# Kernel optimization log

Measured on AMD Instinct MI355X. Metric: run time of the kernel, lower is better.

Reference implementation:

```python
import jax, jax.numpy as jnp
import numpy as np

B, L, H, F = 8, 1024, 512, 4

def setup_inputs() -> dict:
    key = jax.random.key(0)
    ks = jax.random.split(key, 5)
    x = jax.random.normal(ks[0], (B, L, H), dtype=jnp.float32)
    x_mask = jax.random.randint(ks[1], (B, L), 0, 2).astype(jnp.int32)
    W_proj = jax.random.normal(ks[2], (H, H * F), dtype=jnp.float32) * (1.0 / np.sqrt(H))
    b_proj = jnp.zeros((H * F,), dtype=jnp.float32)
    W_gate = jax.random.normal(ks[3], (2 * H, 2 * H), dtype=jnp.float32) * (1.0 / np.sqrt(2 * H))
    b_gate = jnp.zeros((2 * H,), dtype=jnp.float32)
    return {"x": x, "x_mask": x_mask, "W_proj": W_proj, "b_proj": b_proj,
            "W_gate": W_gate, "b_gate": b_gate}

def masked_softmax(logits, mask, eps=1e-13):
    # allennlp-style masked softmax used throughout sgnlp:
    # softmax(logits * mask) * mask, renormalized.
    m = mask.astype(logits.dtype)
    p = jax.nn.softmax(logits * m, axis=-1) * m
    return p / (p.sum(axis=-1, keepdims=True) + eps)

def reference(x, x_mask, W_proj, b_proj, W_gate, b_gate):
    b, l, h = x.shape
    # multi-factor projection: (B,L,H) -> (B,L,H,F) with relu (Linear activation='relu', dropout=0)
    y = jax.nn.relu(jnp.einsum('blh,hk->blk', x, W_proj) + b_proj)
    y = y.reshape(b, l, h, F)
    # per-factor self-attn scores stacked on last axis: (B,L,L,F)
    scores = jnp.einsum('blhf,bmhf->blmf', y, y)
    self_attn = scores.max(axis=-1)  # attn_pooling == 'max'
    # pairwise mask, zero diagonal
    mask = x_mask[:, :, None] * x_mask[:, None, :]
    mask = mask * (1 - jnp.eye(l, dtype=mask.dtype))
    alpha = masked_softmax(self_attn, mask)
    multi_attn_enc = jnp.einsum('blm,bmh->blh', alpha, x)
    joint = jnp.concatenate([x, multi_attn_enc], axis=-1)  # (B,L,2H)
    gate = jax.nn.sigmoid(jnp.einsum('blk,kj->blj', joint, W_gate) + b_gate)
    return gate * joint
```

## Files before the change

### kernel.cpp

```cpp
#include <hip/hip_runtime.h>


typedef _Float16 half8 __attribute__((ext_vector_type(8)));
typedef float floatx4 __attribute__((ext_vector_type(4)));

typedef const __attribute__((address_space(1))) void* gas_ptr;
typedef __attribute__((address_space(3))) void* las_ptr;


template<int NCH, int NT>
__device__ __forceinline__ void init_ptrs(const _Float16* src, int row0, int ld,
                                          const _Float16* gp[NCH]) {
  int t = threadIdx.x;
#pragma unroll
  for (int p = 0; p < NCH; ++p) {
    int c = p * NT + t;
    int row = c >> 3;
    int kg = c & 7;
    int gk = (kg ^ (row & 7)) << 3;
    gp[p] = src + (size_t)(row0 + row) * ld + gk;
  }
}

template<int NCH, int NT>
__device__ __forceinline__ void stage(const _Float16* const gp[NCH], _Float16* ldsbuf) {
  int t = threadIdx.x;
#pragma unroll
  for (int p = 0; p < NCH; ++p)
    __builtin_amdgcn_global_load_lds((gas_ptr)gp[p],
                                     (las_ptr)(ldsbuf + t * 8 + p * NT * 8), 16, 0, 0);
}

template<int NCH>
__device__ __forceinline__ void bump(const _Float16* gp[NCH], int d) {
#pragma unroll
  for (int p = 0; p < NCH; ++p) gp[p] += d;
}

__device__ __forceinline__ half8 frag_ld(const _Float16* lds, int row, int g) {
  return *(const half8*)(lds + row * 64 + ((g ^ (row & 7)) << 3));
}

__device__ __forceinline__ void mfma_tile44(const _Float16* lds_a, const _Float16* lds_b,
                                            floatx4 acc[4][4], int wm, int wn,
                                            int l16, int quad) {
#pragma unroll
  for (int kf = 0; kf < 2; ++kf) {
    half8 af[4], bf[4];
#pragma unroll
    for (int i = 0; i < 4; ++i) af[i] = frag_ld(lds_a, wm * 64 + i * 16 + l16, kf * 4 + quad);
#pragma unroll
    for (int i = 0; i < 4; ++i) bf[i] = frag_ld(lds_b, wn * 64 + i * 16 + l16, kf * 4 + quad);
#pragma unroll
    for (int mi = 0; mi < 4; ++mi)
#pragma unroll
      for (int ni = 0; ni < 4; ++ni)
        acc[mi][ni] = __builtin_amdgcn_mfma_f32_16x16x32_f16(af[mi], bf[ni], acc[mi][ni], 0, 0, 0);
  }
}

#define ZERO_ACC44(acc)                                 \
  _Pragma("unroll") for (int mi = 0; mi < 4; ++mi)      \
  _Pragma("unroll") for (int ni = 0; ni < 4; ++ni)      \
  _Pragma("unroll") for (int r = 0; r < 4; ++r) acc[mi][ni][r] = 0.0f;

__device__ __forceinline__ void mfma_tile42(const _Float16* la, const _Float16* lb,
                                            floatx4 acc[4][2], int wm, int wn,
                                            int l16, int quad) {
#pragma unroll
  for (int kf = 0; kf < 2; ++kf) {
    half8 af[4], bf[2];
#pragma unroll
    for (int i = 0; i < 4; ++i) af[i] = frag_ld(la, wm * 64 + i * 16 + l16, kf * 4 + quad);
#pragma unroll
    for (int i = 0; i < 2; ++i) bf[i] = frag_ld(lb, wn * 32 + i * 16 + l16, kf * 4 + quad);
#pragma unroll
    for (int mi = 0; mi < 4; ++mi)
#pragma unroll
      for (int ni = 0; ni < 2; ++ni)
        acc[mi][ni] = __builtin_amdgcn_mfma_f32_16x16x32_f16(af[mi], bf[ni], acc[mi][ni], 0, 0, 0);
  }
}

#define ZERO_ACC42(acc)                                 \
  _Pragma("unroll") for (int mi = 0; mi < 4; ++mi)      \
  _Pragma("unroll") for (int ni = 0; ni < 2; ++ni)      \
  _Pragma("unroll") for (int r = 0; r < 4; ++r) acc[mi][ni][r] = 0.0f;


__global__ void x_prep_kernel(const float* __restrict__ in, _Float16* __restrict__ x16,
                              _Float16* __restrict__ xT) {
  __shared__ float tile[32][33];
  const int R = 1024, C = 512;
  int c0 = blockIdx.y * 32, r0 = blockIdx.z * 32;
  size_t boff = (size_t)blockIdx.x * R * C;
  in += boff; x16 += boff; xT += boff;
  int tx = threadIdx.x & 31, ty = threadIdx.x >> 5;
#pragma unroll
  for (int i = 0; i < 32; i += 8) {
    float v = in[(size_t)(r0 + ty + i) * C + c0 + tx];
    tile[ty + i][tx] = v;
    x16[(size_t)(r0 + ty + i) * C + c0 + tx] = (_Float16)v;
  }
  __syncthreads();
#pragma unroll
  for (int i = 0; i < 32; i += 8)
    xT[(size_t)(c0 + ty + i) * R + r0 + tx] = (_Float16)tile[tx][ty + i];
}

__global__ void w_prep_kernel(const float* __restrict__ Wp, _Float16* __restrict__ WpT,
                              const float* __restrict__ Wg, _Float16* __restrict__ WgT) {
  __shared__ float tile[32][33];
  const float* in; _Float16* out; int R, C, c0, r0;
  if (blockIdx.z == 0) {
    in = Wp; out = WpT; R = 512; C = 2048;
    c0 = blockIdx.x * 32; r0 = blockIdx.y * 32;
  } else {
    in = Wg; out = WgT; R = 1024; C = 1024;
    c0 = (blockIdx.x & 31) * 32; r0 = (blockIdx.y * 2 + (blockIdx.x >> 5)) * 32;
  }
  int tx = threadIdx.x & 31, ty = threadIdx.x >> 5;
#pragma unroll
  for (int i = 0; i < 32; i += 8)
    tile[ty + i][tx] = in[(size_t)(r0 + ty + i) * C + c0 + tx];
  __syncthreads();
#pragma unroll
  for (int i = 0; i < 32; i += 8) {
    int rr = c0 + ty + i;
    int prow = (blockIdx.z == 0) ? ((rr & 3) * 512 + (rr >> 2)) : rr;
    out[(size_t)prow * R + r0 + tx] = (_Float16)tile[tx][ty + i];
  }
}


__global__ __launch_bounds__(256) void proj_kernel(const _Float16* __restrict__ x16,
                                                   const _Float16* __restrict__ WpT,
                                                   const float* __restrict__ bp,
                                                   _Float16* __restrict__ y_t) {
  __shared__ __align__(16) _Float16 ldsA[2][128 * 64];
  __shared__ __align__(16) _Float16 ldsB[2][128 * 64];
  int id = blockIdx.x;
  int xcd = id & 7, r = id >> 3;
  int i0 = (xcd * 8 + (r & 7)) * 128;
  int n0 = (r >> 3) * 128;
  int t = threadIdx.x, lane = t & 63, w = t >> 6;
  int wm = w >> 1, wn = w & 1, quad = lane >> 4, l16 = lane & 15;
  const _Float16* gpA[4]; const _Float16* gpB[4];
  init_ptrs<4, 256>(x16, i0, 512, gpA);
  init_ptrs<4, 256>(WpT, n0, 512, gpB);
  floatx4 acc[4][4];
  ZERO_ACC44(acc);
  stage<4, 256>(gpA, ldsA[0]); bump<4>(gpA, 64);
  stage<4, 256>(gpB, ldsB[0]); bump<4>(gpB, 64);
#pragma unroll 1
  for (int kt = 0; kt < 8; ++kt) {
    __syncthreads();
    if (kt < 7) {
      stage<4, 256>(gpA, ldsA[(kt + 1) & 1]); bump<4>(gpA, 64);
      stage<4, 256>(gpB, ldsB[(kt + 1) & 1]); bump<4>(gpB, 64);
    }
    mfma_tile44(ldsA[kt & 1], ldsB[kt & 1], acc, wm, wn, l16, quad);
  }
#pragma unroll
  for (int mi = 0; mi < 4; ++mi)
#pragma unroll
    for (int ni = 0; ni < 4; ++ni)
#pragma unroll
      for (int r2 = 0; r2 < 4; ++r2) {
        int gr = i0 + wm * 64 + mi * 16 + quad * 4 + r2;
        int gc = n0 + wn * 64 + ni * 16 + l16;
        int f = gc >> 9, h = gc & 511;
        float c = fmaxf(acc[mi][ni][r2] + bp[h * 4 + f], 0.0f);
        int b = gr >> 10, l = gr & 1023;
        y_t[(((size_t)(b * 4 + f)) * 1024 + l) * 512 + h] = (_Float16)c;
      }
}


__global__ __launch_bounds__(256, 3) void score_kernel(const _Float16* __restrict__ y_t,
                                                       float* __restrict__ S) {
  __shared__ __align__(16) char smem[49152];
  _Float16* LA0 = (_Float16*)smem;
  _Float16* LA1 = (_Float16*)(smem + 16384);
  _Float16* LB0 = (_Float16*)(smem + 32768);
  _Float16* LB1 = (_Float16*)(smem + 40960);
  int id = blockIdx.x;
  int b = id & 7;
  int tt = id >> 3;
  int ti = 0;
  while (tt >= 16 - 2 * ti) { tt -= 16 - 2 * ti; ++ti; }
  int jh = 2 * ti + tt;
  int i0 = ti * 128, j0 = jh * 64;
  int t = threadIdx.x, lane = t & 63, w = t >> 6;
  int wm = w >> 1, wn = w & 1, quad = lane >> 4, l16 = lane & 15;
  const int PLANE = 1024 * 512;
  const _Float16* base = y_t + (size_t)b * 4 * PLANE;
  const _Float16* gpA[4]; const _Float16* gpB[2];
  init_ptrs<4, 256>(base, i0, 512, gpA);
  init_ptrs<2, 256>(base, j0, 512, gpB);
  floatx4 acc[4][2], smax[4][2];
  ZERO_ACC42(acc);
  stage<4, 256>(gpA, LA0); bump<4>(gpA, 64);
  stage<2, 256>(gpB, LB0); bump<2>(gpB, 64);
#pragma unroll 1
  for (int f = 0; f < 4; ++f) {
#pragma unroll 1
    for (int kt = 0; kt < 8; ++kt) {
      __syncthreads();
      if (f * 8 + kt < 31) {
        if (kt == 7) { bump<4>(gpA, PLANE - 512); bump<2>(gpB, PLANE - 512); }
        stage<4, 256>(gpA, ((kt + 1) & 1) ? LA1 : LA0); bump<4>(gpA, 64);
        stage<2, 256>(gpB, ((kt + 1) & 1) ? LB1 : LB0); bump<2>(gpB, 64);
      }
      mfma_tile42((kt & 1) ? LA1 : LA0, (kt & 1) ? LB1 : LB0, acc, wm, wn, l16, quad);
    }
    if (f == 0) {
#pragma unroll
      for (int mi = 0; mi < 4; ++mi)
#pragma unroll
        for (int ni = 0; ni < 2; ++ni) smax[mi][ni] = acc[mi][ni];
    } else {
#pragma unroll
      for (int mi = 0; mi < 4; ++mi)
#pragma unroll
        for (int ni = 0; ni < 2; ++ni)
#pragma unroll
          for (int r = 0; r < 4; ++r)
            smax[mi][ni][r] = fmaxf(smax[mi][ni][r], acc[mi][ni][r]);
    }
    ZERO_ACC42(acc);
  }
  float* Sb = S + (size_t)b * 1024 * 1024;
#pragma unroll
  for (int mi = 0; mi < 4; ++mi)
#pragma unroll
    for (int ni = 0; ni < 2; ++ni)
#pragma unroll
      for (int r = 0; r < 4; ++r) {
        int gi = i0 + wm * 64 + mi * 16 + quad * 4 + r;
        int gj = j0 + wn * 32 + ni * 16 + l16;
        Sb[(size_t)gi * 1024 + gj] = smax[mi][ni][r];
      }
  if (jh >= 2 * ti + 2) {
    __syncthreads();
    float* tl = (float*)smem;
#pragma unroll
    for (int mi = 0; mi < 4; ++mi)
#pragma unroll
      for (int ni = 0; ni < 2; ++ni)
#pragma unroll
        for (int r = 0; r < 4; ++r)
          tl[(wm * 64 + mi * 16 + quad * 4 + r) * 65 + (wn * 32 + ni * 16 + l16)] =
              smax[mi][ni][r];
    __syncthreads();
#pragma unroll 1
    for (int k = 0; k < 32; ++k) {
      int flat = k * 256 + t;
      int rm = flat >> 7, cm = flat & 127;
      Sb[(size_t)(j0 + rm) * 1024 + (i0 + cm)] = tl[cm * 65 + rm];
    }
  }
}


__global__ __launch_bounds__(256) void softmax_kernel(const float* __restrict__ S,
                                                      const int* __restrict__ xmask,
                                                      _Float16* __restrict__ alpha) {
  __shared__ float red[16];
  int id = blockIdx.x;
  int b = id & 7, l = id >> 3;
  int row = b * 1024 + l;
  const float* sr = S + (size_t)row * 1024;
  const int* mr = xmask + b * 1024;
  int t = threadIdx.x, lane = t & 63, wid = t >> 6;
  int rm = mr[l];
  float v[4], mm[4];
  float vmax = 0.0f;
#pragma unroll
  for (int q = 0; q < 4; ++q) {
    int i = t + q * 256;
    int m = (rm && mr[i] && (i != l)) ? 1 : 0;
    mm[q] = (float)m;
    v[q] = m ? sr[i] : 0.0f;
    vmax = fmaxf(vmax, v[q]);
  }
  for (int off = 32; off; off >>= 1) vmax = fmaxf(vmax, __shfl_down(vmax, off));
  if (lane == 0) red[wid] = vmax;
  __syncthreads();
  if (t == 0) red[8] = fmaxf(fmaxf(red[0], red[1]), fmaxf(red[2], red[3]));
  __syncthreads();
  vmax = red[8];
  float e[4], E = 0.0f, E2 = 0.0f;
#pragma unroll
  for (int q = 0; q < 4; ++q) {
    e[q] = expf(v[q] - vmax);
    E += e[q];
    E2 += e[q] * mm[q];
  }
  for (int off = 32; off; off >>= 1) {
    E += __shfl_down(E, off);
    E2 += __shfl_down(E2, off);
  }
  if (lane == 0) { red[wid] = E; red[4 + wid] = E2; }
  __syncthreads();
  if (t == 0) {
    red[9] = red[0] + red[1] + red[2] + red[3];
    red[10] = red[4] + red[5] + red[6] + red[7];
  }
  __syncthreads();
  E = red[9]; E2 = red[10];
  float inv = 1.0f / (E2 + 1e-13f * E);
  _Float16* ar = alpha + (size_t)row * 1024;
#pragma unroll
  for (int q = 0; q < 4; ++q) {
    int i = t + q * 256;
    ar[i] = (_Float16)(e[q] * mm[q] * inv);
  }
}


__global__ __launch_bounds__(256) void attn_kernel(const _Float16* __restrict__ alpha,
                                                   const _Float16* __restrict__ xT,
                                                   _Float16* __restrict__ enc) {
  __shared__ __align__(16) _Float16 ldsA[2][64 * 64];
  __shared__ __align__(16) _Float16 ldsB[2][128 * 64];
  int id = blockIdx.x;
  int b = id & 7;
  int r2 = id >> 3;
  int i0 = (r2 >> 2) * 64;
  int n0 = (r2 & 3) * 128;
  const _Float16* A = alpha + (size_t)b * 1024 * 1024;
  const _Float16* Bm = xT + (size_t)b * 512 * 1024;
  int t = threadIdx.x, lane = t & 63, wn = t >> 6;
  int quad = lane >> 4, l16 = lane & 15;
  const _Float16* gpA[2]; const _Float16* gpB[4];
  init_ptrs<2, 256>(A, i0, 1024, gpA);
  init_ptrs<4, 256>(Bm, n0, 1024, gpB);
  floatx4 acc[4][2];
  ZERO_ACC42(acc);
  stage<2, 256>(gpA, ldsA[0]); bump<2>(gpA, 64);
  stage<4, 256>(gpB, ldsB[0]); bump<4>(gpB, 64);
#pragma unroll 1
  for (int kt = 0; kt < 16; ++kt) {
    __syncthreads();
    if (kt < 15) {
      stage<2, 256>(gpA, ldsA[(kt + 1) & 1]); bump<2>(gpA, 64);
      stage<4, 256>(gpB, ldsB[(kt + 1) & 1]); bump<4>(gpB, 64);
    }
    const _Float16* la = ldsA[kt & 1];
    const _Float16* lb = ldsB[kt & 1];
#pragma unroll
    for (int kf = 0; kf < 2; ++kf) {
      half8 af[4], bf[2];
#pragma unroll
      for (int i = 0; i < 4; ++i) af[i] = frag_ld(la, i * 16 + l16, kf * 4 + quad);
#pragma unroll
      for (int i = 0; i < 2; ++i) bf[i] = frag_ld(lb, wn * 32 + i * 16 + l16, kf * 4 + quad);
#pragma unroll
      for (int mi = 0; mi < 4; ++mi)
#pragma unroll
        for (int ni = 0; ni < 2; ++ni)
          acc[mi][ni] = __builtin_amdgcn_mfma_f32_16x16x32_f16(af[mi], bf[ni], acc[mi][ni], 0, 0, 0);
    }
  }
  _Float16* eb = enc + (size_t)b * 1024 * 512;
#pragma unroll
  for (int mi = 0; mi < 4; ++mi)
#pragma unroll
    for (int ni = 0; ni < 2; ++ni)
#pragma unroll
      for (int r = 0; r < 4; ++r) {
        int gr = i0 + mi * 16 + quad * 4 + r;
        int gc = n0 + wn * 32 + ni * 16 + l16;
        eb[(size_t)gr * 512 + gc] = (_Float16)acc[mi][ni][r];
      }
}


__global__ __launch_bounds__(256) void gate_kernel(const _Float16* __restrict__ x16,
                                                   const _Float16* __restrict__ enc,
                                                   const _Float16* __restrict__ WgT,
                                                   const float* __restrict__ bg,
                                                   float* __restrict__ out) {
  __shared__ __align__(16) _Float16 ldsA[2][128 * 64];
  __shared__ __align__(16) _Float16 ldsB[2][128 * 64];
  int id = blockIdx.x;
  int xcd = id & 7, r = id >> 3;
  int i0 = (xcd * 8 + (r & 7)) * 128;
  int n0 = (r >> 3) * 128;
  int t = threadIdx.x, lane = t & 63, w = t >> 6;
  int wm = w >> 1, wn = w & 1, quad = lane >> 4, l16 = lane & 15;
  const _Float16* gpA[4]; const _Float16* gpA2[4]; const _Float16* gpB[4];
  init_ptrs<4, 256>(x16, i0, 512, gpA);
  init_ptrs<4, 256>(enc, i0, 512, gpA2);
  init_ptrs<4, 256>(WgT, n0, 1024, gpB);
  floatx4 acc[4][4];
  ZERO_ACC44(acc);
  stage<4, 256>(gpA, ldsA[0]); bump<4>(gpA, 64);
  stage<4, 256>(gpB, ldsB[0]); bump<4>(gpB, 64);
#pragma unroll 1
  for (int kt = 0; kt < 16; ++kt) {
    __syncthreads();
    if (kt < 15) {
      if (kt < 7) { stage<4, 256>(gpA,  ldsA[(kt + 1) & 1]); bump<4>(gpA, 64); }
      else        { stage<4, 256>(gpA2, ldsA[(kt + 1) & 1]); bump<4>(gpA2, 64); }
      stage<4, 256>(gpB, ldsB[(kt + 1) & 1]); bump<4>(gpB, 64);
    }
    mfma_tile44(ldsA[kt & 1], ldsB[kt & 1], acc, wm, wn, l16, quad);
  }
#pragma unroll
  for (int mi = 0; mi < 4; ++mi)
#pragma unroll
    for (int ni = 0; ni < 4; ++ni)
#pragma unroll
      for (int r2 = 0; r2 < 4; ++r2) {
        int gr = i0 + wm * 64 + mi * 16 + quad * 4 + r2;
        int gc = n0 + wn * 64 + ni * 16 + l16;
        float c = acc[mi][ni][r2] + bg[gc];
        float g = 1.0f / (1.0f + expf(-c));
        float jv = (gc < 512) ? (float)x16[(size_t)gr * 512 + gc]
                              : (float)enc[(size_t)gr * 512 + (gc - 512)];
        out[(size_t)gr * 1024 + gc] = g * jv;
      }
}


extern "C" void kernel_launch(void* const* d_in, const int* in_sizes, int n_in,
                              void* d_out, int out_size, void* d_ws, size_t ws_size,
                              hipStream_t stream) {
  const float* x  = (const float*)d_in[0];
  const int* xm   = (const int*)d_in[1];
  const float* Wp = (const float*)d_in[2];
  const float* bp = (const float*)d_in[3];
  const float* Wg = (const float*)d_in[4];
  const float* bg = (const float*)d_in[5];
  float* out = (float*)d_out;

  char* ws = (char*)d_ws;
  const size_t MB = 1024 * 1024;
  _Float16* x16 = (_Float16*)(ws);
  _Float16* xT  = (_Float16*)(ws + 8 * MB);
  _Float16* WpT = (_Float16*)(ws + 16 * MB);
  _Float16* WgT = (_Float16*)(ws + 18 * MB);
  _Float16* y_t = (_Float16*)(ws + 20 * MB);
  float*    S   = (float*)(ws + 52 * MB);
  _Float16* alpha = (_Float16*)(ws + 20 * MB);
  _Float16* enc   = (_Float16*)(ws + 36 * MB);

  x_prep_kernel<<<dim3(8, 16, 32), 256, 0, stream>>>(x, x16, xT);
  w_prep_kernel<<<dim3(64, 16, 2), 256, 0, stream>>>(Wp, WpT, Wg, WgT);

  proj_kernel<<<1024, 256, 0, stream>>>(x16, WpT, bp, y_t);
  score_kernel<<<576, 256, 0, stream>>>(y_t, S);
  softmax_kernel<<<8192, 256, 0, stream>>>(S, xm, alpha);
  attn_kernel<<<512, 256, 0, stream>>>(alpha, xT, enc);
  gate_kernel<<<512, 256, 0, stream>>>(x16, enc, WgT, bg, out);
}
```

Baseline: 203.0 us.

## Deepen proj/gate GEMM pipelines to 4-stage K=32 buffers and merge prep kernels

The proj and gate GEMMs move from a double-buffered K=64 LDS scheme to a four-buffer K=32 ring with a paired-row swizzle. They use explicit vmcnt waits and raw barriers so up to three tiles of loads stay in flight, and raise MFMA priority with setprio during compute. The two preprocessing kernels are merged into one launch. This aims to hide global-load latency and cut one launch. In exchange it adds more barriers per K and hand-tuned waitcnt logic that must match the number of outstanding loads.

```diff
diff --git a/kernel.cpp b/kernel.cpp
--- a/kernel.cpp
+++ b/kernel.cpp
@@ -6,6 +6,8 @@
 
 typedef const __attribute__((address_space(1))) void* gas_ptr;
 typedef __attribute__((address_space(3))) void* las_ptr;
+
+#define WAITV(n) asm volatile("s_waitcnt vmcnt(" #n ") lgkmcnt(0)" ::: "memory")
 
 
 template<int NCH, int NT>
@@ -22,6 +24,22 @@
   }
 }
 
+
+template<int NCH, int NT>
+__device__ __forceinline__ void init_ptrs32(const _Float16* src, int row0, int ld,
+                                            const _Float16* gp[NCH]) {
+  int t = threadIdx.x;
+#pragma unroll
+  for (int p = 0; p < NCH; ++p) {
+    int c = p * NT + t;
+    int pair = c >> 3, s = c & 7;
+    int q = s ^ (pair & 7);
+    int row = row0 + pair * 2 + (q >> 2);
+    int gk = (q & 3) << 3;
+    gp[p] = src + (size_t)row * ld + gk;
+  }
+}
+
 template<int NCH, int NT>
 __device__ __forceinline__ void stage(const _Float16* const gp[NCH], _Float16* ldsbuf) {
   int t = threadIdx.x;
@@ -41,20 +59,42 @@
   return *(const half8*)(lds + row * 64 + ((g ^ (row & 7)) << 3));
 }
 
-__device__ __forceinline__ void mfma_tile44(const _Float16* lds_a, const _Float16* lds_b,
-                                            floatx4 acc[4][4], int wm, int wn,
+__device__ __forceinline__ half8 frag_ld32(const _Float16* lds, int row, int kg) {
+  int pair = row >> 1;
+  int slot = (kg | ((row & 1) << 2)) ^ (pair & 7);
+  return *(const half8*)(lds + pair * 64 + slot * 8);
+}
+
+__device__ __forceinline__ void kstep44(const _Float16* la, const _Float16* lb,
+                                        floatx4 (&acc)[4][4], int ra, int rb, int quad) {
+  half8 af[4], bf[4];
+#pragma unroll
+  for (int mi = 0; mi < 4; ++mi) af[mi] = frag_ld32(la, ra + mi * 16, quad);
+#pragma unroll
+  for (int ni = 0; ni < 4; ++ni) bf[ni] = frag_ld32(lb, rb + ni * 16, quad);
+  __builtin_amdgcn_s_setprio(1);
+#pragma unroll
+  for (int mi = 0; mi < 4; ++mi)
+#pragma unroll
+    for (int ni = 0; ni < 4; ++ni)
+      acc[mi][ni] = __builtin_amdgcn_mfma_f32_16x16x32_f16(af[mi], bf[ni], acc[mi][ni], 0, 0, 0);
+  __builtin_amdgcn_s_setprio(0);
+}
+
+__device__ __forceinline__ void mfma_tile42(const _Float16* la, const _Float16* lb,
+                                            floatx4 acc[4][2], int wm, int wn,
                                             int l16, int quad) {
 #pragma unroll
   for (int kf = 0; kf < 2; ++kf) {
-    half8 af[4], bf[4];
-#pragma unroll
-    for (int i = 0; i < 4; ++i) af[i] = frag_ld(lds_a, wm * 64 + i * 16 + l16, kf * 4 + quad);
-#pragma unroll
-    for (int i = 0; i < 4; ++i) bf[i] = frag_ld(lds_b, wn * 64 + i * 16 + l16, kf * 4 + quad);
+    half8 af[4], bf[2];
+#pragma unroll
+    for (int i = 0; i < 4; ++i) af[i] = frag_ld(la, wm * 64 + i * 16 + l16, kf * 4 + quad);
+#pragma unroll
+    for (int i = 0; i < 2; ++i) bf[i] = frag_ld(lb, wn * 32 + i * 16 + l16, kf * 4 + quad);
 #pragma unroll
     for (int mi = 0; mi < 4; ++mi)
 #pragma unroll
-      for (int ni = 0; ni < 4; ++ni)
+      for (int ni = 0; ni < 2; ++ni)
         acc[mi][ni] = __builtin_amdgcn_mfma_f32_16x16x32_f16(af[mi], bf[ni], acc[mi][ni], 0, 0, 0);
   }
 }
@@ -64,103 +104,100 @@
   _Pragma("unroll") for (int ni = 0; ni < 4; ++ni)      \
   _Pragma("unroll") for (int r = 0; r < 4; ++r) acc[mi][ni][r] = 0.0f;
 
-__device__ __forceinline__ void mfma_tile42(const _Float16* la, const _Float16* lb,
-                                            floatx4 acc[4][2], int wm, int wn,
-                                            int l16, int quad) {
-#pragma unroll
-  for (int kf = 0; kf < 2; ++kf) {
-    half8 af[4], bf[2];
-#pragma unroll
-    for (int i = 0; i < 4; ++i) af[i] = frag_ld(la, wm * 64 + i * 16 + l16, kf * 4 + quad);
-#pragma unroll
-    for (int i = 0; i < 2; ++i) bf[i] = frag_ld(lb, wn * 32 + i * 16 + l16, kf * 4 + quad);
-#pragma unroll
-    for (int mi = 0; mi < 4; ++mi)
-#pragma unroll
-      for (int ni = 0; ni < 2; ++ni)
-        acc[mi][ni] = __builtin_amdgcn_mfma_f32_16x16x32_f16(af[mi], bf[ni], acc[mi][ni], 0, 0, 0);
-  }
-}
-
 #define ZERO_ACC42(acc)                                 \
   _Pragma("unroll") for (int mi = 0; mi < 4; ++mi)      \
   _Pragma("unroll") for (int ni = 0; ni < 2; ++ni)      \
   _Pragma("unroll") for (int r = 0; r < 4; ++r) acc[mi][ni][r] = 0.0f;
 
 
-__global__ void x_prep_kernel(const float* __restrict__ in, _Float16* __restrict__ x16,
-                              _Float16* __restrict__ xT) {
+__global__ __launch_bounds__(256) void prep_kernel(const float* __restrict__ xin,
+                                                   _Float16* __restrict__ x16,
+                                                   _Float16* __restrict__ xT,
+                                                   const float* __restrict__ Wp,
+                                                   _Float16* __restrict__ WpT,
+                                                   const float* __restrict__ Wg,
+                                                   _Float16* __restrict__ WgT) {
   __shared__ float tile[32][33];
-  const int R = 1024, C = 512;
-  int c0 = blockIdx.y * 32, r0 = blockIdx.z * 32;
-  size_t boff = (size_t)blockIdx.x * R * C;
-  in += boff; x16 += boff; xT += boff;
+  int id = blockIdx.x;
   int tx = threadIdx.x & 31, ty = threadIdx.x >> 5;
-#pragma unroll
-  for (int i = 0; i < 32; i += 8) {
-    float v = in[(size_t)(r0 + ty + i) * C + c0 + tx];
-    tile[ty + i][tx] = v;
-    x16[(size_t)(r0 + ty + i) * C + c0 + tx] = (_Float16)v;
-  }
-  __syncthreads();
-#pragma unroll
-  for (int i = 0; i < 32; i += 8)
-    xT[(size_t)(c0 + ty + i) * R + r0 + tx] = (_Float16)tile[tx][ty + i];
-}
-
-__global__ void w_prep_kernel(const float* __restrict__ Wp, _Float16* __restrict__ WpT,
-                              const float* __restrict__ Wg, _Float16* __restrict__ WgT) {
-  __shared__ float tile[32][33];
-  const float* in; _Float16* out; int R, C, c0, r0;
-  if (blockIdx.z == 0) {
-    in = Wp; out = WpT; R = 512; C = 2048;
-    c0 = blockIdx.x * 32; r0 = blockIdx.y * 32;
+  if (id < 4096) {
+    const int R = 1024, C = 512;
+    int b = id & 7, rest = id >> 3;
+    int c0 = (rest & 15) * 32, r0 = (rest >> 4) * 32;
+    size_t boff = (size_t)b * R * C;
+    const float* in = xin + boff;
+    _Float16* o16 = x16 + boff;
+    _Float16* oT = xT + boff;
+#pragma unroll
+    for (int i = 0; i < 32; i += 8) {
+      float v = in[(size_t)(r0 + ty + i) * C + c0 + tx];
+      tile[ty + i][tx] = v;
+      o16[(size_t)(r0 + ty + i) * C + c0 + tx] = (_Float16)v;
+    }
+    __syncthreads();
+#pragma unroll
+    for (int i = 0; i < 32; i += 8)
+      oT[(size_t)(c0 + ty + i) * R + r0 + tx] = (_Float16)tile[tx][ty + i];
   } else {
-    in = Wg; out = WgT; R = 1024; C = 1024;
-    c0 = (blockIdx.x & 31) * 32; r0 = (blockIdx.y * 2 + (blockIdx.x >> 5)) * 32;
-  }
-  int tx = threadIdx.x & 31, ty = threadIdx.x >> 5;
-#pragma unroll
-  for (int i = 0; i < 32; i += 8)
-    tile[ty + i][tx] = in[(size_t)(r0 + ty + i) * C + c0 + tx];
-  __syncthreads();
-#pragma unroll
-  for (int i = 0; i < 32; i += 8) {
-    int rr = c0 + ty + i;
-    int prow = (blockIdx.z == 0) ? ((rr & 3) * 512 + (rr >> 2)) : rr;
-    out[(size_t)prow * R + r0 + tx] = (_Float16)tile[tx][ty + i];
-  }
-}
-
-
-__global__ __launch_bounds__(256) void proj_kernel(const _Float16* __restrict__ x16,
-                                                   const _Float16* __restrict__ WpT,
-                                                   const float* __restrict__ bp,
-                                                   _Float16* __restrict__ y_t) {
-  __shared__ __align__(16) _Float16 ldsA[2][128 * 64];
-  __shared__ __align__(16) _Float16 ldsB[2][128 * 64];
+    int w = id - 4096;
+    int bx = w & 63, by = (w >> 6) & 15, bz = w >> 10;
+    const float* in; _Float16* out; int R, C, c0, r0;
+    if (bz == 0) {
+      in = Wp; out = WpT; R = 512; C = 2048;
+      c0 = bx * 32; r0 = by * 32;
+    } else {
+      in = Wg; out = WgT; R = 1024; C = 1024;
+      c0 = (bx & 31) * 32; r0 = (by * 2 + (bx >> 5)) * 32;
+    }
+#pragma unroll
+    for (int i = 0; i < 32; i += 8)
+      tile[ty + i][tx] = in[(size_t)(r0 + ty + i) * C + c0 + tx];
+    __syncthreads();
+#pragma unroll
+    for (int i = 0; i < 32; i += 8) {
+      int rr = c0 + ty + i;
+      int prow = (bz == 0) ? ((rr & 3) * 512 + (rr >> 2)) : rr;
+      out[(size_t)prow * R + r0 + tx] = (_Float16)tile[tx][ty + i];
+    }
+  }
+}
+
+
+__global__ __launch_bounds__(256, 2) void proj_kernel(const _Float16* __restrict__ x16,
+                                                      const _Float16* __restrict__ WpT,
+                                                      const float* __restrict__ bp,
+                                                      _Float16* __restrict__ y_t) {
+  __shared__ __align__(16) _Float16 ldsA[4][128 * 32];
+  __shared__ __align__(16) _Float16 ldsB[4][128 * 32];
   int id = blockIdx.x;
   int xcd = id & 7, r = id >> 3;
   int i0 = (xcd * 8 + (r & 7)) * 128;
   int n0 = (r >> 3) * 128;
   int t = threadIdx.x, lane = t & 63, w = t >> 6;
   int wm = w >> 1, wn = w & 1, quad = lane >> 4, l16 = lane & 15;
-  const _Float16* gpA[4]; const _Float16* gpB[4];
-  init_ptrs<4, 256>(x16, i0, 512, gpA);
-  init_ptrs<4, 256>(WpT, n0, 512, gpB);
+  int ra = wm * 64 + l16, rb = wn * 64 + l16;
+  const _Float16* gpA[2]; const _Float16* gpB[2];
+  init_ptrs32<2, 256>(x16, i0, 512, gpA);
+  init_ptrs32<2, 256>(WpT, n0, 512, gpB);
   floatx4 acc[4][4];
   ZERO_ACC44(acc);
-  stage<4, 256>(gpA, ldsA[0]); bump<4>(gpA, 64);
-  stage<4, 256>(gpB, ldsB[0]); bump<4>(gpB, 64);
+  stage<2, 256>(gpA, ldsA[0]); bump<2>(gpA, 32);
+  stage<2, 256>(gpB, ldsB[0]); bump<2>(gpB, 32);
+  stage<2, 256>(gpA, ldsA[1]); bump<2>(gpA, 32);
+  stage<2, 256>(gpB, ldsB[1]); bump<2>(gpB, 32);
+  stage<2, 256>(gpA, ldsA[2]); bump<2>(gpA, 32);
+  stage<2, 256>(gpB, ldsB[2]); bump<2>(gpB, 32);
 #pragma unroll 1
-  for (int kt = 0; kt < 8; ++kt) {
-    __syncthreads();
-    if (kt < 7) {
-      stage<4, 256>(gpA, ldsA[(kt + 1) & 1]); bump<4>(gpA, 64);
-      stage<4, 256>(gpB, ldsB[(kt + 1) & 1]); bump<4>(gpB, 64);
-    }
-    mfma_tile44(ldsA[kt & 1], ldsB[kt & 1], acc, wm, wn, l16, quad);
-  }
+  for (int u = 0; u < 13; ++u) {
+    WAITV(8);
+    __builtin_amdgcn_s_barrier();
+    stage<2, 256>(gpA, ldsA[(u + 3) & 3]); bump<2>(gpA, 32);
+    stage<2, 256>(gpB, ldsB[(u + 3) & 3]); bump<2>(gpB, 32);
+    kstep44(ldsA[u & 3], ldsB[u & 3], acc, ra, rb, quad);
+  }
+  WAITV(8); __builtin_amdgcn_s_barrier(); kstep44(ldsA[1], ldsB[1], acc, ra, rb, quad);
+  WAITV(4); __builtin_amdgcn_s_barrier(); kstep44(ldsA[2], ldsB[2], acc, ra, rb, quad);
+  WAITV(0); __builtin_amdgcn_s_barrier(); kstep44(ldsA[3], ldsB[3], acc, ra, rb, quad);
 #pragma unroll
   for (int mi = 0; mi < 4; ++mi)
 #pragma unroll
@@ -377,37 +414,45 @@
 }
 
 
-__global__ __launch_bounds__(256) void gate_kernel(const _Float16* __restrict__ x16,
-                                                   const _Float16* __restrict__ enc,
-                                                   const _Float16* __restrict__ WgT,
-                                                   const float* __restrict__ bg,
-                                                   float* __restrict__ out) {
-  __shared__ __align__(16) _Float16 ldsA[2][128 * 64];
-  __shared__ __align__(16) _Float16 ldsB[2][128 * 64];
+__global__ __launch_bounds__(256, 2) void gate_kernel(const _Float16* __restrict__ x16,
+                                                      const _Float16* __restrict__ enc,
+                                                      const _Float16* __restrict__ WgT,
+                                                      const float* __restrict__ bg,
+                                                      float* __restrict__ out) {
+  __shared__ __align__(16) _Float16 ldsA[4][128 * 32];
+  __shared__ __align__(16) _Float16 ldsB[4][128 * 32];
   int id = blockIdx.x;
   int xcd = id & 7, r = id >> 3;
   int i0 = (xcd * 8 + (r & 7)) * 128;
   int n0 = (r >> 3) * 128;
   int t = threadIdx.x, lane = t & 63, w = t >> 6;
   int wm = w >> 1, wn = w & 1, quad = lane >> 4, l16 = lane & 15;
-  const _Float16* gpA[4]; const _Float16* gpA2[4]; const _Float16* gpB[4];
-  init_ptrs<4, 256>(x16, i0, 512, gpA);
-  init_ptrs<4, 256>(enc, i0, 512, gpA2);
-  init_ptrs<4, 256>(WgT, n0, 1024, gpB);
+  int ra = wm * 64 + l16, rb = wn * 64 + l16;
+  const _Float16* gpA[2]; const _Float16* gpA2[2]; const _Float16* gpB[2];
+  init_ptrs32<2, 256>(x16, i0, 512, gpA);
+  init_ptrs32<2, 256>(enc, i0, 512, gpA2);
+  init_ptrs32<2, 256>(WgT, n0, 1024, gpB);
   floatx4 acc[4][4];
   ZERO_ACC44(acc);
-  stage<4, 256>(gpA, ldsA[0]); bump<4>(gpA, 64);
-  stage<4, 256>(gpB, ldsB[0]); bump<4>(gpB, 64);
+  stage<2, 256>(gpA, ldsA[0]); bump<2>(gpA, 32);
+  stage<2, 256>(gpB, ldsB[0]); bump<2>(gpB, 32);
+  stage<2, 256>(gpA, ldsA[1]); bump<2>(gpA, 32);
+  stage<2, 256>(gpB, ldsB[1]); bump<2>(gpB, 32);
+  stage<2, 256>(gpA, ldsA[2]); bump<2>(gpA, 32);
+  stage<2, 256>(gpB, ldsB[2]); bump<2>(gpB, 32);
 #pragma unroll 1
-  for (int kt = 0; kt < 16; ++kt) {
-    __syncthreads();
-    if (kt < 15) {
-      if (kt < 7) { stage<4, 256>(gpA,  ldsA[(kt + 1) & 1]); bump<4>(gpA, 64); }
-      else        { stage<4, 256>(gpA2, ldsA[(kt + 1) & 1]); bump<4>(gpA2, 64); }
-      stage<4, 256>(gpB, ldsB[(kt + 1) & 1]); bump<4>(gpB, 64);
-    }
-    mfma_tile44(ldsA[kt & 1], ldsB[kt & 1], acc, wm, wn, l16, quad);
-  }
+  for (int u = 0; u < 29; ++u) {
+    WAITV(8);
+    __builtin_amdgcn_s_barrier();
+    int v = u + 3;
+    if (v < 16) { stage<2, 256>(gpA,  ldsA[v & 3]); bump<2>(gpA, 32); }
+    else        { stage<2, 256>(gpA2, ldsA[v & 3]); bump<2>(gpA2, 32); }
+    stage<2, 256>(gpB, ldsB[v & 3]); bump<2>(gpB, 32);
+    kstep44(ldsA[u & 3], ldsB[u & 3], acc, ra, rb, quad);
+  }
+  WAITV(8); __builtin_amdgcn_s_barrier(); kstep44(ldsA[1], ldsB[1], acc, ra, rb, quad);
+  WAITV(4); __builtin_amdgcn_s_barrier(); kstep44(ldsA[2], ldsB[2], acc, ra, rb, quad);
+  WAITV(0); __builtin_amdgcn_s_barrier(); kstep44(ldsA[3], ldsB[3], acc, ra, rb, quad);
 #pragma unroll
   for (int mi = 0; mi < 4; ++mi)
 #pragma unroll
@@ -447,8 +492,7 @@
   _Float16* alpha = (_Float16*)(ws + 20 * MB);
   _Float16* enc   = (_Float16*)(ws + 36 * MB);
 
-  x_prep_kernel<<<dim3(8, 16, 32), 256, 0, stream>>>(x, x16, xT);
-  w_prep_kernel<<<dim3(64, 16, 2), 256, 0, stream>>>(Wp, WpT, Wg, WgT);
+  prep_kernel<<<6144, 256, 0, stream>>>(x, x16, xT, Wp, WpT, Wg, WgT);
 
   proj_kernel<<<1024, 256, 0, stream>>>(x16, WpT, bp, y_t);
   score_kernel<<<576, 256, 0, stream>>>(y_t, S);
```

Result: slower. 213.5 us (+5.2%).
